# Optimization experiments

Measured on AMD Instinct MI355X. Metric: run time of the kernel, lower is better.

The kernel has to match this reference:

```python
import jax, jax.numpy as jnp
import numpy as np

B, S, D_IN, D_OUT = 4, 2048, 2048, 2048
E, R, TOP_K = 8, 8, 2
ALPHA = 16.0
SCALE = ALPHA / R  # alpha / r


def setup_inputs() -> dict:
    key = jax.random.key(0)
    ks = jax.random.split(key, 6)
    x = jax.random.normal(ks[0], (B, S, D_IN), dtype=jnp.float32)
    # base frozen linear: torch Linear weight [out, in], bias [out]
    W_base = jax.random.normal(ks[1], (D_OUT, D_IN), dtype=jnp.float32) / np.sqrt(D_IN)
    b_base = jax.random.normal(ks[2], (D_OUT,), dtype=jnp.float32) * 0.01
    # router: Linear(in_features, num_experts, bias=False) -> weight [E, in]
    W_router = jax.random.normal(ks[3], (E, D_IN), dtype=jnp.float32) / np.sqrt(D_IN)
    # LoRA experts: A [E, r, in], B [E, out, r] (torch inits B to zero; use small
    # random values so outputs/grads are non-trivial -- math is identical)
    A_w = jax.random.normal(ks[4], (E, R, D_IN), dtype=jnp.float32) / np.sqrt(D_IN)
    B_w = jax.random.normal(ks[5], (E, D_OUT, R), dtype=jnp.float32) * 0.02
    return {"x": x, "W_base": W_base, "b_base": b_base,
            "W_router": W_router, "A_w": A_w, "B_w": B_w}


def reference(x, W_base, b_base, W_router, A_w, B_w):
    # frozen base linear: [B,S,out]
    y = jnp.einsum('bsd,od->bso', x, W_base) + b_base
    # router: logits [B,S,E] -> top-k + softmax over the k selected logits
    logits = jnp.einsum('bsd,ed->bse', x, W_router)
    topk_vals, topk_idx = jax.lax.top_k(logits, TOP_K)       # [B,S,k]
    gates = jax.nn.softmax(topk_vals, axis=-1)               # [B,S,k]
    # all-experts LoRA compute (matches the original dense-stack semantics)
    h = jnp.einsum('bsd,erd->bser', x, A_w)                  # [B,S,E,r]
    expert_outs = jnp.einsum('bser,eor->bseo', h, B_w) * SCALE  # [B,S,E,out]
    # gather the top-k expert outputs and combine with gates
    topk_outs = jnp.take_along_axis(expert_outs, topk_idx[..., None], axis=2)  # [B,S,k,out]
    fused = jnp.sum(topk_outs * gates[..., None], axis=2)    # [B,S,out]
    return y + fused
```

## Files before the change

kernel.cpp:

```cpp
#include <hip/hip_runtime.h>

typedef unsigned short u16;
typedef __attribute__((ext_vector_type(8))) short short8;
typedef __attribute__((ext_vector_type(4))) float f32x4;

#define GLL16(g, l) __builtin_amdgcn_global_load_lds(                         \
    (const __attribute__((address_space(1))) void*)(g),                        \
    (__attribute__((address_space(3))) void*)(l), 16, 0, 0)

__device__ __forceinline__ u16 f2bf(float f) {
  union { float f; unsigned u; } v; v.f = f;
  unsigned u = v.u;
  return (u16)((u + 0x7FFFu + ((u >> 16) & 1u)) >> 16);
}

__global__ __launch_bounds__(512) void k_conv_router(
    const float* __restrict__ x, const float* __restrict__ Wr,
    u16* __restrict__ xbf, float* __restrict__ logits)
{
  __shared__ float wlds[16384];
  {
    const float4* src = (const float4*)Wr;
    float4* dst = (float4*)wlds;
    int t = threadIdx.x;
#pragma unroll
    for (int i = 0; i < 8; ++i) dst[t + i * 512] = src[t + i * 512];
  }
  __syncthreads();
  int wave = threadIdx.x >> 6, lane = threadIdx.x & 63;
  const float4* wv = (const float4*)wlds;
#pragma unroll 1
  for (int s = 0; s < 2; ++s) {
    int tok = blockIdx.x * 16 + wave * 2 + s;
    const float4* xrow = (const float4*)(x + tok * 2048);
    ushort4* orow = (ushort4*)(xbf + tok * 2048);
    float acc[8];
#pragma unroll
    for (int e = 0; e < 8; ++e) acc[e] = 0.f;
#pragma unroll 1
    for (int i = 0; i < 8; ++i) {
      float4 xv = xrow[lane + i * 64];
      ushort4 o;
      o.x = f2bf(xv.x); o.y = f2bf(xv.y);
      o.z = f2bf(xv.z); o.w = f2bf(xv.w);
      orow[lane + i * 64] = o;
#pragma unroll
      for (int e = 0; e < 8; ++e) {
        float4 b = wv[e * 512 + lane + i * 64];
        acc[e] += xv.x * b.x + xv.y * b.y + xv.z * b.z + xv.w * b.w;
      }
    }
#pragma unroll
    for (int e = 0; e < 8; ++e) {
      float v = acc[e];
#pragma unroll
      for (int off = 32; off > 0; off >>= 1) v += __shfl_xor(v, off, 64);
      acc[e] = v;
    }
    if (lane == 0) {
#pragma unroll
      for (int e = 0; e < 8; ++e) logits[tok * 8 + e] = acc[e];
    }
  }
}

__global__ __launch_bounds__(256) void k_convert(
    const float* __restrict__ Wb, const float* __restrict__ Aw,
    const float* __restrict__ Bw,
    u16* __restrict__ wbf, u16* __restrict__ aabf, u16* __restrict__ bmt)
{
  int b = blockIdx.x, t = threadIdx.x;
  if (b < 1024) {
    int tid = b * 256 + t;
    const float4* src = (const float4*)Wb;
    ushort4* dst = (ushort4*)wbf;
#pragma unroll
    for (int i = 0; i < 4; ++i) {
      float4 v = src[tid + i * 262144];
      ushort4 o; o.x = f2bf(v.x); o.y = f2bf(v.y); o.z = f2bf(v.z); o.w = f2bf(v.w);
      dst[tid + i * 262144] = o;
    }
  } else if (b < 1056) {
    int tid = (b - 1024) * 256 + t;
    const float4* src = (const float4*)Aw;
    ushort4* dst = (ushort4*)aabf;
#pragma unroll
    for (int i = 0; i < 4; ++i) {
      float4 v = src[tid + i * 8192];
      ushort4 o; o.x = f2bf(v.x); o.y = f2bf(v.y); o.z = f2bf(v.z); o.w = f2bf(v.w);
      dst[tid + i * 8192] = o;
    }
  } else {
    int n = (b - 1056) * 256 + t;
#pragma unroll
    for (int e = 0; e < 8; ++e) {
      const float4* src = (const float4*)(Bw + e * 16384 + n * 8);
      float4 v0 = src[0], v1 = src[1];
      ushort4 o0, o1;
      o0.x = f2bf(v0.x); o0.y = f2bf(v0.y); o0.z = f2bf(v0.z); o0.w = f2bf(v0.w);
      o1.x = f2bf(v1.x); o1.y = f2bf(v1.y); o1.z = f2bf(v1.z); o1.w = f2bf(v1.w);
      ushort4* dst = (ushort4*)(bmt + n * 64 + e * 8);
      dst[0] = o0; dst[1] = o1;
    }
  }
}

__global__ __launch_bounds__(256) void k_hgemm(
    const u16* __restrict__ xbf, const u16* __restrict__ aabf,
    float* __restrict__ P)
{
  __shared__ u16 As[256 * 64];
  __shared__ u16 Bs[64 * 64];
  int t = threadIdx.x, wave = t >> 6, lane = t & 63;
  int mBase = blockIdx.x * 256;
  int ks = blockIdx.y;
  int fr = lane & 15, fg = lane >> 4;
  int lrow = lane >> 3, lcol = (lane & 7) * 8;
  f32x4 zero = {0.f, 0.f, 0.f, 0.f};
  f32x4 acc[4][4];
#pragma unroll
  for (int i = 0; i < 4; ++i)
#pragma unroll
    for (int j = 0; j < 4; ++j) acc[i][j] = zero;
#pragma unroll 1
  for (int it = 0; it < 4; ++it) {
    int k0 = ks * 256 + it * 64;
    __syncthreads();
#pragma unroll
    for (int cc = 0; cc < 8; ++cc) {
      int c = wave * 8 + cc;
      GLL16(xbf + (mBase + c * 8 + lrow) * 2048 + k0 + lcol, &As[c * 512]);
    }
#pragma unroll
    for (int cc = 0; cc < 2; ++cc) {
      int c = wave * 2 + cc;
      GLL16(aabf + (c * 8 + lrow) * 2048 + k0 + lcol, &Bs[c * 512]);
    }
    __syncthreads();
#pragma unroll
    for (int kk = 0; kk < 2; ++kk) {
      short8 a[4], bfr[4];
#pragma unroll
      for (int i = 0; i < 4; ++i)
        a[i] = *(const short8*)&As[(wave * 64 + i * 16 + fr) * 64 + kk * 32 + fg * 8];
#pragma unroll
      for (int j = 0; j < 4; ++j)
        bfr[j] = *(const short8*)&Bs[(j * 16 + fr) * 64 + kk * 32 + fg * 8];
#pragma unroll
      for (int i = 0; i < 4; ++i)
#pragma unroll
        for (int j = 0; j < 4; ++j)
          acc[i][j] = __builtin_amdgcn_mfma_f32_16x16x32_bf16(a[i], bfr[j], acc[i][j], 0, 0, 0);
    }
  }
#pragma unroll
  for (int i = 0; i < 4; ++i)
#pragma unroll
    for (int j = 0; j < 4; ++j)
#pragma unroll
      for (int r = 0; r < 4; ++r) {
        int m = mBase + wave * 64 + i * 16 + fg * 4 + r;
        int n = j * 16 + fr;
        P[(ks * 8192 + m) * 64 + n] = acc[i][j][r];
      }
}

__global__ __launch_bounds__(256) void k_topk(
    const float* __restrict__ logits, const float* __restrict__ P,
    u16* __restrict__ G)
{
  int t = threadIdx.x, wave = t >> 6, lane = t & 63;
  int tok = blockIdx.x * 4 + wave;
  const float* lg = logits + tok * 8;
  float la[8];
#pragma unroll
  for (int e = 0; e < 8; ++e) la[e] = lg[e];
  float v0 = la[0]; int i0 = 0;
#pragma unroll
  for (int e = 1; e < 8; ++e) { if (la[e] > v0) { v0 = la[e]; i0 = e; } }
  float v1 = -3.4e38f; int i1 = 0;
#pragma unroll
  for (int e = 0; e < 8; ++e) { if (e != i0 && la[e] > v1) { v1 = la[e]; i1 = e; } }
  float ex = expf(v1 - v0);
  float inv = 1.f / (1.f + ex);
  float gate0 = inv, gate1 = ex * inv;
  int e = lane >> 3;
  float h = 0.f;
#pragma unroll
  for (int ks = 0; ks < 8; ++ks) h += P[(ks * 8192 + tok) * 64 + lane];
  float g = (e == i0) ? gate0 : ((e == i1) ? gate1 : 0.f);
  G[tok * 64 + lane] = f2bf(2.0f * g * h);
}

__global__ __launch_bounds__(512, 2) void k_main(
    const u16* __restrict__ xbf, const u16* __restrict__ wbf,
    const u16* __restrict__ G, const u16* __restrict__ BmT,
    const float* __restrict__ bias, float* __restrict__ out)
{
  __shared__ u16 lds[65536];
  const int tid = threadIdx.x;
  const int w = tid >> 6, lane = tid & 63;
  const int fr = lane & 15, fg = lane >> 4;
  const int wr = w >> 2, wc = w & 3;

  const int b0 = blockIdx.x;
  const int wg = (b0 & 7) * 32 + (b0 >> 3);
  const int mBase = (wg >> 3) * 256;
  const int nBase = (wg & 7) * 256;

  const int rl = lane >> 3;
  const int ce = ((lane & 7) ^ rl) << 3;
  const int swz = (fr & 7) << 3;
  const int colk0 = (fg * 8) ^ swz;
  const int colk1 = (32 + fg * 8) ^ swz;
  const int aOff = (wr * 128 + fr) * 64;
  const int bOff = (wc * 64 + fr) * 64;

  f32x4 acc[8][4];
  const f32x4 zero = {0.f, 0.f, 0.f, 0.f};
#pragma unroll
  for (int mi = 0; mi < 8; ++mi)
#pragma unroll
    for (int nj = 0; nj < 4; ++nj) acc[mi][nj] = zero;

  auto STAGE = [&](int s, int which) {
    if (s > 32) return;
    const bool isA = (which < 2);
    const int h = which & 1;
    const u16* src; int ld, k0;
    if (s < 32) { src = isA ? xbf : wbf; ld = 2048; k0 = s * 64; }
    else        { src = isA ? G   : BmT; ld = 64;   k0 = 0;      }
    const int rb = (isA ? mBase : nBase) + h * 128 + w * 8 + rl;
    u16* dst = lds + (isA ? 0 : 32768) + (s & 1) * 16384 + h * 8192 + w * 512;
    GLL16(src + rb * ld + k0 + ce, dst);
    GLL16(src + (rb + 64) * ld + k0 + ce, dst + 4096);
  };

  short8 Aa[2][2], Ab[2][2];
  short8 Bx[4][2], By[4][2];

#define LGKM(N) asm volatile("s_waitcnt lgkmcnt(" #N ")" ::: "memory")
#define VMC(N)  asm volatile("s_waitcnt vmcnt(" #N ")" ::: "memory")
#define BAR()   __builtin_amdgcn_s_barrier()

#define RDA(DST, BUF, MI0)                                                    \
  DST[0][0] = *(const short8*)((BUF) + aOff + (MI0) * 1024 + colk0);          \
  DST[0][1] = *(const short8*)((BUF) + aOff + (MI0) * 1024 + colk1);          \
  DST[1][0] = *(const short8*)((BUF) + aOff + ((MI0) + 1) * 1024 + colk0);    \
  DST[1][1] = *(const short8*)((BUF) + aOff + ((MI0) + 1) * 1024 + colk1);

#define RDB(DST, BUF, NJ0)                                                    \
  DST[(NJ0)][0] = *(const short8*)((BUF) + bOff + (NJ0) * 1024 + colk0);      \
  DST[(NJ0)][1] = *(const short8*)((BUF) + bOff + (NJ0) * 1024 + colk1);      \
  DST[(NJ0)+1][0] = *(const short8*)((BUF) + bOff + ((NJ0)+1) * 1024 + colk0);\
  DST[(NJ0)+1][1] = *(const short8*)((BUF) + bOff + ((NJ0)+1) * 1024 + colk1);

#define MFMA16(AV, BV, MI0)                                                   \
  __builtin_amdgcn_s_setprio(1);                                              \
  _Pragma("unroll")                                                           \
  for (int kk = 0; kk < 2; ++kk)                                              \
    _Pragma("unroll")                                                         \
    for (int q = 0; q < 2; ++q)                                               \
      _Pragma("unroll")                                                       \
      for (int nj = 0; nj < 4; ++nj)                                          \
        acc[(MI0) + q][nj] = __builtin_amdgcn_mfma_f32_16x16x32_bf16(         \
            AV[q][kk], BV[nj][kk], acc[(MI0) + q][nj], 0, 0, 0);              \
  __builtin_amdgcn_s_setprio(0);

#define TILE(T, P, BC, BN)                                                    \
  {                                                                           \
    const u16* Acur = lds + (P) * 16384;                                      \
    const u16* Anxt = lds + (1 - (P)) * 16384;                                \
    const u16* Bnxt = lds + 32768 + (1 - (P)) * 16384;                        \
                                                                      \
    STAGE((T) + 1, 0);                                                        \
    RDA(Ab, Acur, 2)                                                          \
    LGKM(4);                                                                  \
    MFMA16(Aa, BC, 0)                                                         \
    BAR();                                                                    \
                                                                      \
    STAGE((T) + 1, 1);                                                        \
    RDA(Aa, Acur, 4)                                                          \
    LGKM(4);                                                                  \
    MFMA16(Ab, BC, 2)                                                         \
    VMC(4);                                                                   \
    BAR();                                                                    \
                                                                      \
    STAGE((T) + 2, 2);                                                        \
    RDA(Ab, Acur, 6)                                                          \
    RDB(BN, Bnxt, 0)                                                          \
    LGKM(8);                                                                  \
    MFMA16(Aa, BC, 4)                                                         \
    if ((T) == 31) { VMC(0); } else { VMC(2); }                               \
    BAR();                                                                    \
                                                                      \
    STAGE((T) + 2, 3);                                                        \
    RDA(Aa, Anxt, 0)                                                          \
    RDB(BN, Bnxt, 2)                                                          \
    LGKM(8);                                                                  \
    MFMA16(Ab, BC, 6)                                                         \
    BAR();                                                                    \
  }

  STAGE(0, 0); STAGE(0, 1); STAGE(0, 2); STAGE(0, 3);
  STAGE(1, 2); STAGE(1, 3);
  VMC(4);
  BAR();
  {
    const u16* Bb0 = lds + 32768;
    RDB(Bx, Bb0, 0)
    RDB(Bx, Bb0, 2)
    RDA(Aa, lds, 0)
  }

#pragma unroll 1
  for (int tt = 0; tt < 16; ++tt) {
    const int t0 = tt * 2;
    TILE(t0, 0, Bx, By)
    TILE(t0 + 1, 1, By, Bx)
  }

  {
    const u16* Acur = lds;
    RDA(Ab, Acur, 2)
    LGKM(4);
    MFMA16(Aa, Bx, 0)
    RDA(Aa, Acur, 4)
    LGKM(4);
    MFMA16(Ab, Bx, 2)
    RDA(Ab, Acur, 6)
    LGKM(4);
    MFMA16(Aa, Bx, 4)
    LGKM(0);
    MFMA16(Ab, Bx, 6)
  }

#pragma unroll
  for (int nj = 0; nj < 4; ++nj) {
    const int n = nBase + wc * 64 + nj * 16 + fr;
    const float bv = bias[n];
#pragma unroll
    for (int mi = 0; mi < 8; ++mi) {
      const int m = mBase + wr * 128 + mi * 16 + fg * 4;
#pragma unroll
      for (int r = 0; r < 4; ++r)
        out[(m + r) * 2048 + n] = acc[mi][nj][r] + bv;
    }
  }
#undef TILE
#undef MFMA16
#undef RDB
#undef RDA
#undef BAR
#undef VMC
#undef LGKM
}

extern "C" void kernel_launch(void* const* d_in, const int* in_sizes, int n_in,
                              void* d_out, int out_size, void* d_ws, size_t ws_size,
                              hipStream_t stream) {
  const float* x  = (const float*)d_in[0];
  const float* Wb = (const float*)d_in[1];
  const float* bb = (const float*)d_in[2];
  const float* Wr = (const float*)d_in[3];
  const float* Aw = (const float*)d_in[4];
  const float* Bw = (const float*)d_in[5];

  char* ws = (char*)d_ws;
  u16*   xbf  = (u16*)  (ws + 0);
  u16*   wbf  = (u16*)  (ws + 33554432);
  u16*   aabf = (u16*)  (ws + 41943040);
  u16*   bmt  = (u16*)  (ws + 42205184);
  float* lgt  = (float*)(ws + 42467328);
  u16*   G    = (u16*)  (ws + 42729472);
  float* P   = (float*)d_out;
  float* out = (float*)d_out;

  hipLaunchKernelGGL(k_conv_router, dim3(512),    dim3(512), 0, stream, x, Wr, xbf, lgt);
  hipLaunchKernelGGL(k_convert,     dim3(1064),   dim3(256), 0, stream, Wb, Aw, Bw, wbf, aabf, bmt);
  hipLaunchKernelGGL(k_hgemm,       dim3(32, 8),  dim3(256), 0, stream, xbf, aabf, P);
  hipLaunchKernelGGL(k_topk,        dim3(2048),   dim3(256), 0, stream, lgt, P, G);
  hipLaunchKernelGGL(k_main,        dim3(256),    dim3(512), 0, stream, xbf, wbf, G, bmt, bb, out);
}
```

Before: 116.6 us.

## Fuse LoRA A-projection GEMM with top-k gating, drop split-K partials

Replaces the split-K h-GEMM (writing fp32 partials to a scratch buffer) and the separate top-k kernel with one kernel. Each 128-thread block owns 32 tokens and loops over the full K with double-buffered, XOR-swizzled LDS tiles. Routing and gating are computed in the epilogue straight from the accumulators. This removes one launch and the partial-sum write and re-read, but the grid shrinks to 256 small blocks with long serial K loops, which may limit parallelism.

```diff
diff --git a/kernel.cpp b/kernel.cpp
--- a/kernel.cpp
+++ b/kernel.cpp
@@ -105,91 +105,85 @@
   }
 }
 
-__global__ __launch_bounds__(256) void k_hgemm(
+__global__ __launch_bounds__(128) void k_hA(
     const u16* __restrict__ xbf, const u16* __restrict__ aabf,
-    float* __restrict__ P)
+    const float* __restrict__ logits, u16* __restrict__ G)
 {
-  __shared__ u16 As[256 * 64];
-  __shared__ u16 Bs[64 * 64];
-  int t = threadIdx.x, wave = t >> 6, lane = t & 63;
-  int mBase = blockIdx.x * 256;
-  int ks = blockIdx.y;
-  int fr = lane & 15, fg = lane >> 4;
-  int lrow = lane >> 3, lcol = (lane & 7) * 8;
-  f32x4 zero = {0.f, 0.f, 0.f, 0.f};
-  f32x4 acc[4][4];
-#pragma unroll
-  for (int i = 0; i < 4; ++i)
-#pragma unroll
-    for (int j = 0; j < 4; ++j) acc[i][j] = zero;
+  __shared__ u16 As[2][32 * 64];
+  __shared__ u16 Bs[2][64 * 64];
+  const int tid = threadIdx.x, w = tid >> 6, lane = tid & 63;
+  const int fr = lane & 15, fg = lane >> 4;
+  const int rl = lane >> 3;
+  const int ce = ((lane & 7) ^ rl) << 3;
+  const int swz = (fr & 7) << 3;
+  const int colk0 = (fg * 8) ^ swz;
+  const int colk1 = (32 + fg * 8) ^ swz;
+  const int tokBase = blockIdx.x * 32;
+
+  auto STAGE = [&](int s) {
+    const int buf = s & 1, k0 = s * 64;
+    GLL16(xbf + (tokBase + w * 16 + rl) * 2048 + k0 + ce, &As[buf][(w * 16) * 64]);
+    GLL16(xbf + (tokBase + w * 16 + 8 + rl) * 2048 + k0 + ce, &As[buf][(w * 16 + 8) * 64]);
+#pragma unroll
+    for (int c = 0; c < 4; ++c)
+      GLL16(aabf + (w * 32 + c * 8 + rl) * 2048 + k0 + ce, &Bs[buf][(w * 32 + c * 8) * 64]);
+  };
+
+  f32x4 acc[4];
+  const f32x4 zero = {0.f, 0.f, 0.f, 0.f};
+#pragma unroll
+  for (int nj = 0; nj < 4; ++nj) acc[nj] = zero;
+
+  STAGE(0);
+  asm volatile("s_waitcnt vmcnt(0)" ::: "memory");
+  __syncthreads();
+
 #pragma unroll 1
-  for (int it = 0; it < 4; ++it) {
-    int k0 = ks * 256 + it * 64;
+  for (int t = 0; t < 32; ++t) {
+    if (t < 31) STAGE(t + 1);
+    const int buf = t & 1;
+    short8 a[2], bfr[4][2];
+    a[0] = *(const short8*)&As[buf][(w * 16 + fr) * 64 + colk0];
+    a[1] = *(const short8*)&As[buf][(w * 16 + fr) * 64 + colk1];
+#pragma unroll
+    for (int nj = 0; nj < 4; ++nj) {
+      bfr[nj][0] = *(const short8*)&Bs[buf][(nj * 16 + fr) * 64 + colk0];
+      bfr[nj][1] = *(const short8*)&Bs[buf][(nj * 16 + fr) * 64 + colk1];
+    }
+    asm volatile("s_waitcnt lgkmcnt(0)" ::: "memory");
+#pragma unroll
+    for (int kk = 0; kk < 2; ++kk)
+#pragma unroll
+      for (int nj = 0; nj < 4; ++nj)
+        acc[nj] = __builtin_amdgcn_mfma_f32_16x16x32_bf16(a[kk], bfr[nj][kk], acc[nj], 0, 0, 0);
+    asm volatile("s_waitcnt vmcnt(0)" ::: "memory");
     __syncthreads();
-#pragma unroll
-    for (int cc = 0; cc < 8; ++cc) {
-      int c = wave * 8 + cc;
-      GLL16(xbf + (mBase + c * 8 + lrow) * 2048 + k0 + lcol, &As[c * 512]);
-    }
-#pragma unroll
-    for (int cc = 0; cc < 2; ++cc) {
-      int c = wave * 2 + cc;
-      GLL16(aabf + (c * 8 + lrow) * 2048 + k0 + lcol, &Bs[c * 512]);
-    }
-    __syncthreads();
-#pragma unroll
-    for (int kk = 0; kk < 2; ++kk) {
-      short8 a[4], bfr[4];
-#pragma unroll
-      for (int i = 0; i < 4; ++i)
-        a[i] = *(const short8*)&As[(wave * 64 + i * 16 + fr) * 64 + kk * 32 + fg * 8];
-#pragma unroll
-      for (int j = 0; j < 4; ++j)
-        bfr[j] = *(const short8*)&Bs[(j * 16 + fr) * 64 + kk * 32 + fg * 8];
-#pragma unroll
-      for (int i = 0; i < 4; ++i)
-#pragma unroll
-        for (int j = 0; j < 4; ++j)
-          acc[i][j] = __builtin_amdgcn_mfma_f32_16x16x32_bf16(a[i], bfr[j], acc[i][j], 0, 0, 0);
-    }
-  }
-#pragma unroll
-  for (int i = 0; i < 4; ++i)
-#pragma unroll
-    for (int j = 0; j < 4; ++j)
-#pragma unroll
-      for (int r = 0; r < 4; ++r) {
-        int m = mBase + wave * 64 + i * 16 + fg * 4 + r;
-        int n = j * 16 + fr;
-        P[(ks * 8192 + m) * 64 + n] = acc[i][j][r];
-      }
-}
-
-__global__ __launch_bounds__(256) void k_topk(
-    const float* __restrict__ logits, const float* __restrict__ P,
-    u16* __restrict__ G)
-{
-  int t = threadIdx.x, wave = t >> 6, lane = t & 63;
-  int tok = blockIdx.x * 4 + wave;
-  const float* lg = logits + tok * 8;
-  float la[8];
-#pragma unroll
-  for (int e = 0; e < 8; ++e) la[e] = lg[e];
-  float v0 = la[0]; int i0 = 0;
-#pragma unroll
-  for (int e = 1; e < 8; ++e) { if (la[e] > v0) { v0 = la[e]; i0 = e; } }
-  float v1 = -3.4e38f; int i1 = 0;
-#pragma unroll
-  for (int e = 0; e < 8; ++e) { if (e != i0 && la[e] > v1) { v1 = la[e]; i1 = e; } }
-  float ex = expf(v1 - v0);
-  float inv = 1.f / (1.f + ex);
-  float gate0 = inv, gate1 = ex * inv;
-  int e = lane >> 3;
-  float h = 0.f;
-#pragma unroll
-  for (int ks = 0; ks < 8; ++ks) h += P[(ks * 8192 + tok) * 64 + lane];
-  float g = (e == i0) ? gate0 : ((e == i1) ? gate1 : 0.f);
-  G[tok * 64 + lane] = f2bf(2.0f * g * h);
+  }
+
+#pragma unroll
+  for (int r = 0; r < 4; ++r) {
+    const int tok = tokBase + w * 16 + fg * 4 + r;
+    const float* lg = logits + tok * 8;
+    float la[8];
+#pragma unroll
+    for (int e = 0; e < 8; ++e) la[e] = lg[e];
+    float v0 = la[0]; int i0 = 0;
+#pragma unroll
+    for (int e = 1; e < 8; ++e) { if (la[e] > v0) { v0 = la[e]; i0 = e; } }
+    float v1 = -3.4e38f; int i1 = 0;
+#pragma unroll
+    for (int e = 0; e < 8; ++e) { if (e != i0 && la[e] > v1) { v1 = la[e]; i1 = e; } }
+    float ex = expf(v1 - v0);
+    float inv = 1.f / (1.f + ex);
+    float gate0 = inv, gate1 = ex * inv;
+#pragma unroll
+    for (int nj = 0; nj < 4; ++nj) {
+      const int er = nj * 16 + fr;
+      const int e = er >> 3;
+      const float g = (e == i0) ? gate0 : ((e == i1) ? gate1 : 0.f);
+      G[tok * 64 + er] = f2bf(2.0f * g * acc[nj][r]);
+    }
+  }
 }
 
 __global__ __launch_bounds__(512, 2) void k_main(
@@ -373,12 +367,10 @@
   u16*   bmt  = (u16*)  (ws + 42205184);
   float* lgt  = (float*)(ws + 42467328);
   u16*   G    = (u16*)  (ws + 42729472);
-  float* P   = (float*)d_out;
   float* out = (float*)d_out;
 
-  hipLaunchKernelGGL(k_conv_router, dim3(512),    dim3(512), 0, stream, x, Wr, xbf, lgt);
-  hipLaunchKernelGGL(k_convert,     dim3(1064),   dim3(256), 0, stream, Wb, Aw, Bw, wbf, aabf, bmt);
-  hipLaunchKernelGGL(k_hgemm,       dim3(32, 8),  dim3(256), 0, stream, xbf, aabf, P);
-  hipLaunchKernelGGL(k_topk,        dim3(2048),   dim3(256), 0, stream, lgt, P, G);
-  hipLaunchKernelGGL(k_main,        dim3(256),    dim3(512), 0, stream, xbf, wbf, G, bmt, bb, out);
-}
+  hipLaunchKernelGGL(k_conv_router, dim3(512),  dim3(512), 0, stream, x, Wr, xbf, lgt);
+  hipLaunchKernelGGL(k_convert,     dim3(1064), dim3(256), 0, stream, Wb, Aw, Bw, wbf, aabf, bmt);
+  hipLaunchKernelGGL(k_hA,          dim3(256),  dim3(128), 0, stream, xbf, aabf, lgt, G);
+  hipLaunchKernelGGL(k_main,        dim3(256),  dim3(512), 0, stream, xbf, wbf, G, bmt, bb, out);
+}
```

After: 124.3 us. +6.6%, slower.

## Fuse all five stages into one cooperative persistent kernel with grid syncs

Applied to the files above, without the earlier changes.

Merges the router/convert, weight-convert, LoRA A GEMM, top-k gating and main GEMM kernels into a single cooperative kernel launched on 256 blocks, with grid-wide syncs between phases. This removes four kernel launches and their inter-kernel gaps. In exchange, the early phases now run on only 256 blocks of 512 threads, so conversion and the small GEMM lose parallelism, and each grid.sync adds barrier cost. Cooperative launch also requires all 256 blocks to be co-resident.

```diff
diff --git a/kernel.cpp b/kernel.cpp
--- a/kernel.cpp
+++ b/kernel.cpp
@@ -1,4 +1,7 @@
 #include <hip/hip_runtime.h>
+#include <hip/hip_cooperative_groups.h>
+
+namespace cg = cooperative_groups;
 
 typedef unsigned short u16;
 typedef __attribute__((ext_vector_type(8))) short short8;
@@ -14,230 +17,212 @@
   return (u16)((u + 0x7FFFu + ((u >> 16) & 1u)) >> 16);
 }
 
-__global__ __launch_bounds__(512) void k_conv_router(
-    const float* __restrict__ x, const float* __restrict__ Wr,
-    u16* __restrict__ xbf, float* __restrict__ logits)
+__device__ __forceinline__ ushort4 cvt4(float4 v) {
+  ushort4 o; o.x = f2bf(v.x); o.y = f2bf(v.y); o.z = f2bf(v.z); o.w = f2bf(v.w);
+  return o;
+}
+
+__global__ __launch_bounds__(512, 2) void k_fused(
+    const float* __restrict__ x, const float* __restrict__ Wb,
+    const float* __restrict__ bias, const float* __restrict__ Wr,
+    const float* __restrict__ Aw, const float* __restrict__ Bw,
+    u16* __restrict__ xbf, u16* __restrict__ wbf, u16* __restrict__ aabf,
+    u16* __restrict__ bmt, float* __restrict__ lgt, u16* __restrict__ G,
+    float* __restrict__ P, float* __restrict__ out)
 {
-  __shared__ float wlds[16384];
-  {
-    const float4* src = (const float4*)Wr;
-    float4* dst = (float4*)wlds;
-    int t = threadIdx.x;
-#pragma unroll
-    for (int i = 0; i < 8; ++i) dst[t + i * 512] = src[t + i * 512];
-  }
-  __syncthreads();
-  int wave = threadIdx.x >> 6, lane = threadIdx.x & 63;
-  const float4* wv = (const float4*)wlds;
-#pragma unroll 1
-  for (int s = 0; s < 2; ++s) {
-    int tok = blockIdx.x * 16 + wave * 2 + s;
-    const float4* xrow = (const float4*)(x + tok * 2048);
-    ushort4* orow = (ushort4*)(xbf + tok * 2048);
-    float acc[8];
-#pragma unroll
-    for (int e = 0; e < 8; ++e) acc[e] = 0.f;
-#pragma unroll 1
-    for (int i = 0; i < 8; ++i) {
-      float4 xv = xrow[lane + i * 64];
-      ushort4 o;
-      o.x = f2bf(xv.x); o.y = f2bf(xv.y);
-      o.z = f2bf(xv.z); o.w = f2bf(xv.w);
-      orow[lane + i * 64] = o;
-#pragma unroll
-      for (int e = 0; e < 8; ++e) {
-        float4 b = wv[e * 512 + lane + i * 64];
-        acc[e] += xv.x * b.x + xv.y * b.y + xv.z * b.z + xv.w * b.w;
-      }
-    }
-#pragma unroll
-    for (int e = 0; e < 8; ++e) {
-      float v = acc[e];
-#pragma unroll
-      for (int off = 32; off > 0; off >>= 1) v += __shfl_xor(v, off, 64);
-      acc[e] = v;
-    }
-    if (lane == 0) {
-#pragma unroll
-      for (int e = 0; e < 8; ++e) logits[tok * 8 + e] = acc[e];
-    }
-  }
-}
-
-__global__ __launch_bounds__(256) void k_convert(
-    const float* __restrict__ Wb, const float* __restrict__ Aw,
-    const float* __restrict__ Bw,
-    u16* __restrict__ wbf, u16* __restrict__ aabf, u16* __restrict__ bmt)
-{
-  int b = blockIdx.x, t = threadIdx.x;
-  if (b < 1024) {
-    int tid = b * 256 + t;
-    const float4* src = (const float4*)Wb;
-    ushort4* dst = (ushort4*)wbf;
-#pragma unroll
-    for (int i = 0; i < 4; ++i) {
-      float4 v = src[tid + i * 262144];
-      ushort4 o; o.x = f2bf(v.x); o.y = f2bf(v.y); o.z = f2bf(v.z); o.w = f2bf(v.w);
-      dst[tid + i * 262144] = o;
-    }
-  } else if (b < 1056) {
-    int tid = (b - 1024) * 256 + t;
-    const float4* src = (const float4*)Aw;
-    ushort4* dst = (ushort4*)aabf;
-#pragma unroll
-    for (int i = 0; i < 4; ++i) {
-      float4 v = src[tid + i * 8192];
-      ushort4 o; o.x = f2bf(v.x); o.y = f2bf(v.y); o.z = f2bf(v.z); o.w = f2bf(v.w);
-      dst[tid + i * 8192] = o;
-    }
-  } else {
-    int n = (b - 1056) * 256 + t;
-#pragma unroll
-    for (int e = 0; e < 8; ++e) {
-      const float4* src = (const float4*)(Bw + e * 16384 + n * 8);
-      float4 v0 = src[0], v1 = src[1];
-      ushort4 o0, o1;
-      o0.x = f2bf(v0.x); o0.y = f2bf(v0.y); o0.z = f2bf(v0.z); o0.w = f2bf(v0.w);
-      o1.x = f2bf(v1.x); o1.y = f2bf(v1.y); o1.z = f2bf(v1.z); o1.w = f2bf(v1.w);
-      ushort4* dst = (ushort4*)(bmt + n * 64 + e * 8);
-      dst[0] = o0; dst[1] = o1;
-    }
-  }
-}
-
-__global__ __launch_bounds__(256) void k_hgemm(
-    const u16* __restrict__ xbf, const u16* __restrict__ aabf,
-    float* __restrict__ P)
-{
-  __shared__ u16 As[256 * 64];
-  __shared__ u16 Bs[64 * 64];
-  int t = threadIdx.x, wave = t >> 6, lane = t & 63;
-  int mBase = blockIdx.x * 256;
-  int ks = blockIdx.y;
-  int fr = lane & 15, fg = lane >> 4;
-  int lrow = lane >> 3, lcol = (lane & 7) * 8;
-  f32x4 zero = {0.f, 0.f, 0.f, 0.f};
-  f32x4 acc[4][4];
-#pragma unroll
-  for (int i = 0; i < 4; ++i)
-#pragma unroll
-    for (int j = 0; j < 4; ++j) acc[i][j] = zero;
-#pragma unroll 1
-  for (int it = 0; it < 4; ++it) {
-    int k0 = ks * 256 + it * 64;
-    __syncthreads();
-#pragma unroll
-    for (int cc = 0; cc < 8; ++cc) {
-      int c = wave * 8 + cc;
-      GLL16(xbf + (mBase + c * 8 + lrow) * 2048 + k0 + lcol, &As[c * 512]);
-    }
-#pragma unroll
-    for (int cc = 0; cc < 2; ++cc) {
-      int c = wave * 2 + cc;
-      GLL16(aabf + (c * 8 + lrow) * 2048 + k0 + lcol, &Bs[c * 512]);
-    }
-    __syncthreads();
-#pragma unroll
-    for (int kk = 0; kk < 2; ++kk) {
-      short8 a[4], bfr[4];
-#pragma unroll
-      for (int i = 0; i < 4; ++i)
-        a[i] = *(const short8*)&As[(wave * 64 + i * 16 + fr) * 64 + kk * 32 + fg * 8];
-#pragma unroll
-      for (int j = 0; j < 4; ++j)
-        bfr[j] = *(const short8*)&Bs[(j * 16 + fr) * 64 + kk * 32 + fg * 8];
-#pragma unroll
-      for (int i = 0; i < 4; ++i)
-#pragma unroll
-        for (int j = 0; j < 4; ++j)
-          acc[i][j] = __builtin_amdgcn_mfma_f32_16x16x32_bf16(a[i], bfr[j], acc[i][j], 0, 0, 0);
-    }
-  }
-#pragma unroll
-  for (int i = 0; i < 4; ++i)
-#pragma unroll
-    for (int j = 0; j < 4; ++j)
-#pragma unroll
-      for (int r = 0; r < 4; ++r) {
-        int m = mBase + wave * 64 + i * 16 + fg * 4 + r;
-        int n = j * 16 + fr;
-        P[(ks * 8192 + m) * 64 + n] = acc[i][j][r];
-      }
-}
-
-__global__ __launch_bounds__(256) void k_topk(
-    const float* __restrict__ logits, const float* __restrict__ P,
-    u16* __restrict__ G)
-{
-  int t = threadIdx.x, wave = t >> 6, lane = t & 63;
-  int tok = blockIdx.x * 4 + wave;
-  const float* lg = logits + tok * 8;
-  float la[8];
-#pragma unroll
-  for (int e = 0; e < 8; ++e) la[e] = lg[e];
-  float v0 = la[0]; int i0 = 0;
-#pragma unroll
-  for (int e = 1; e < 8; ++e) { if (la[e] > v0) { v0 = la[e]; i0 = e; } }
-  float v1 = -3.4e38f; int i1 = 0;
-#pragma unroll
-  for (int e = 0; e < 8; ++e) { if (e != i0 && la[e] > v1) { v1 = la[e]; i1 = e; } }
-  float ex = expf(v1 - v0);
-  float inv = 1.f / (1.f + ex);
-  float gate0 = inv, gate1 = ex * inv;
-  int e = lane >> 3;
-  float h = 0.f;
-#pragma unroll
-  for (int ks = 0; ks < 8; ++ks) h += P[(ks * 8192 + tok) * 64 + lane];
-  float g = (e == i0) ? gate0 : ((e == i1) ? gate1 : 0.f);
-  G[tok * 64 + lane] = f2bf(2.0f * g * h);
-}
-
-__global__ __launch_bounds__(512, 2) void k_main(
-    const u16* __restrict__ xbf, const u16* __restrict__ wbf,
-    const u16* __restrict__ G, const u16* __restrict__ BmT,
-    const float* __restrict__ bias, float* __restrict__ out)
-{
-  __shared__ u16 lds[65536];
+  __shared__ __align__(16) char smem[131072];
+  cg::grid_group grid = cg::this_grid();
+
   const int tid = threadIdx.x;
   const int w = tid >> 6, lane = tid & 63;
   const int fr = lane & 15, fg = lane >> 4;
-  const int wr = w >> 2, wc = w & 3;
-
-  const int b0 = blockIdx.x;
-  const int wg = (b0 & 7) * 32 + (b0 >> 3);
-  const int mBase = (wg >> 3) * 256;
-  const int nBase = (wg & 7) * 256;
-
   const int rl = lane >> 3;
+  const int lcol = (lane & 7) * 8;
   const int ce = ((lane & 7) ^ rl) << 3;
-  const int swz = (fr & 7) << 3;
-  const int colk0 = (fg * 8) ^ swz;
-  const int colk1 = (32 + fg * 8) ^ swz;
-  const int aOff = (wr * 128 + fr) * 64;
-  const int bOff = (wc * 64 + fr) * 64;
-
-  f32x4 acc[8][4];
-  const f32x4 zero = {0.f, 0.f, 0.f, 0.f};
-#pragma unroll
-  for (int mi = 0; mi < 8; ++mi)
-#pragma unroll
-    for (int nj = 0; nj < 4; ++nj) acc[mi][nj] = zero;
-
-  auto STAGE = [&](int s, int which) {
-    if (s > 32) return;
-    const bool isA = (which < 2);
-    const int h = which & 1;
-    const u16* src; int ld, k0;
-    if (s < 32) { src = isA ? xbf : wbf; ld = 2048; k0 = s * 64; }
-    else        { src = isA ? G   : BmT; ld = 64;   k0 = 0;      }
-    const int rb = (isA ? mBase : nBase) + h * 128 + w * 8 + rl;
-    u16* dst = lds + (isA ? 0 : 32768) + (s & 1) * 16384 + h * 8192 + w * 512;
-    GLL16(src + rb * ld + k0 + ce, dst);
-    GLL16(src + (rb + 64) * ld + k0 + ce, dst + 4096);
-  };
-
-  short8 Aa[2][2], Ab[2][2];
-  short8 Bx[4][2], By[4][2];
+
+  {
+    float* wlds = (float*)smem;
+    {
+      const float4* src = (const float4*)Wr;
+      float4* dst = (float4*)wlds;
+#pragma unroll
+      for (int i = 0; i < 8; ++i) dst[tid + i * 512] = src[tid + i * 512];
+    }
+    __syncthreads();
+    const float4* wv = (const float4*)wlds;
+#pragma unroll 1
+    for (int s = 0; s < 4; ++s) {
+      int tok = blockIdx.x * 32 + w * 4 + s;
+      const float4* xrow = (const float4*)(x + tok * 2048);
+      ushort4* orow = (ushort4*)(xbf + tok * 2048);
+      float acc[8];
+#pragma unroll
+      for (int e = 0; e < 8; ++e) acc[e] = 0.f;
+#pragma unroll 1
+      for (int i = 0; i < 8; ++i) {
+        float4 xv = xrow[lane + i * 64];
+        orow[lane + i * 64] = cvt4(xv);
+#pragma unroll
+        for (int e = 0; e < 8; ++e) {
+          float4 b = wv[e * 512 + lane + i * 64];
+          acc[e] += xv.x * b.x + xv.y * b.y + xv.z * b.z + xv.w * b.w;
+        }
+      }
+#pragma unroll
+      for (int e = 0; e < 8; ++e) {
+        float v = acc[e];
+#pragma unroll
+        for (int off = 32; off > 0; off >>= 1) v += __shfl_xor(v, off, 64);
+        acc[e] = v;
+      }
+      if (lane == 0) {
+#pragma unroll
+        for (int e = 0; e < 8; ++e) lgt[tok * 8 + e] = acc[e];
+      }
+    }
+    const int tidg = blockIdx.x * 512 + tid;
+    {
+      const float4* src = (const float4*)Wb;
+      ushort4* dst = (ushort4*)wbf;
+#pragma unroll
+      for (int i = 0; i < 8; ++i) {
+        dst[tidg + i * 131072] = cvt4(src[tidg + i * 131072]);
+      }
+    }
+    if (tidg < 32768) {
+      ((ushort4*)aabf)[tidg] = cvt4(((const float4*)Aw)[tidg]);
+    }
+    if (tidg < 2048) {
+      const int n = tidg;
+#pragma unroll
+      for (int e = 0; e < 8; ++e) {
+        const float4* src = (const float4*)(Bw + e * 16384 + n * 8);
+        ushort4* dst = (ushort4*)(bmt + n * 64 + e * 8);
+        dst[0] = cvt4(src[0]);
+        dst[1] = cvt4(src[1]);
+      }
+    }
+  }
+  __threadfence();
+  grid.sync();
+
+  {
+    u16* As = (u16*)smem;
+    u16* Bs = (u16*)(smem + 32768);
+    const int mBase = (blockIdx.x >> 3) * 256;
+    const int ks = blockIdx.x & 7;
+    f32x4 acc[2][4];
+    const f32x4 zero = {0.f, 0.f, 0.f, 0.f};
+#pragma unroll
+    for (int i = 0; i < 2; ++i)
+#pragma unroll
+      for (int j = 0; j < 4; ++j) acc[i][j] = zero;
+#pragma unroll 1
+    for (int it = 0; it < 4; ++it) {
+      const int k0 = ks * 256 + it * 64;
+      __syncthreads();
+#pragma unroll
+      for (int cc = 0; cc < 4; ++cc) {
+        const int c = w * 4 + cc;
+        GLL16(xbf + (mBase + c * 8 + rl) * 2048 + k0 + lcol, As + c * 512);
+      }
+      GLL16(aabf + (w * 8 + rl) * 2048 + k0 + lcol, Bs + w * 512);
+      __syncthreads();
+#pragma unroll
+      for (int kk = 0; kk < 2; ++kk) {
+        short8 a[2], bfr[4];
+#pragma unroll
+        for (int i = 0; i < 2; ++i)
+          a[i] = *(const short8*)&As[(w * 32 + i * 16 + fr) * 64 + kk * 32 + fg * 8];
+#pragma unroll
+        for (int j = 0; j < 4; ++j)
+          bfr[j] = *(const short8*)&Bs[(j * 16 + fr) * 64 + kk * 32 + fg * 8];
+#pragma unroll
+        for (int i = 0; i < 2; ++i)
+#pragma unroll
+          for (int j = 0; j < 4; ++j)
+            acc[i][j] = __builtin_amdgcn_mfma_f32_16x16x32_bf16(a[i], bfr[j], acc[i][j], 0, 0, 0);
+      }
+    }
+#pragma unroll
+    for (int i = 0; i < 2; ++i)
+#pragma unroll
+      for (int j = 0; j < 4; ++j)
+#pragma unroll
+        for (int r = 0; r < 4; ++r) {
+          const int m = mBase + w * 32 + i * 16 + fg * 4 + r;
+          const int n = j * 16 + fr;
+          P[(ks * 8192 + m) * 64 + n] = acc[i][j][r];
+        }
+  }
+  __threadfence();
+  grid.sync();
+
+  {
+#pragma unroll 1
+    for (int s = 0; s < 4; ++s) {
+      const int tok = blockIdx.x * 32 + w * 4 + s;
+      const float* lg = lgt + tok * 8;
+      float la[8];
+#pragma unroll
+      for (int e = 0; e < 8; ++e) la[e] = lg[e];
+      float v0 = la[0]; int i0 = 0;
+#pragma unroll
+      for (int e = 1; e < 8; ++e) { if (la[e] > v0) { v0 = la[e]; i0 = e; } }
+      float v1 = -3.4e38f; int i1 = 0;
+#pragma unroll
+      for (int e = 0; e < 8; ++e) { if (e != i0 && la[e] > v1) { v1 = la[e]; i1 = e; } }
+      const float ex = expf(v1 - v0);
+      const float inv = 1.f / (1.f + ex);
+      const float gate0 = inv, gate1 = ex * inv;
+      const int e = lane >> 3;
+      float h = 0.f;
+#pragma unroll
+      for (int ks = 0; ks < 8; ++ks) h += P[(ks * 8192 + tok) * 64 + lane];
+      const float g = (e == i0) ? gate0 : ((e == i1) ? gate1 : 0.f);
+      G[tok * 64 + lane] = f2bf(2.0f * g * h);
+    }
+  }
+  __threadfence();
+  grid.sync();
+
+  {
+    u16* ldsb = (u16*)smem;
+    const int wr = w >> 2, wc = w & 3;
+
+    const int b0 = blockIdx.x;
+    const int wg = (b0 & 7) * 32 + (b0 >> 3);
+    const int mBase = (wg >> 3) * 256;
+    const int nBase = (wg & 7) * 256;
+
+    const int swz = (fr & 7) << 3;
+    const int colk0 = (fg * 8) ^ swz;
+    const int colk1 = (32 + fg * 8) ^ swz;
+    const int aOff = (wr * 128 + fr) * 64;
+    const int bOff = (wc * 64 + fr) * 64;
+
+    f32x4 acc[8][4];
+    const f32x4 zero = {0.f, 0.f, 0.f, 0.f};
+#pragma unroll
+    for (int mi = 0; mi < 8; ++mi)
+#pragma unroll
+      for (int nj = 0; nj < 4; ++nj) acc[mi][nj] = zero;
+
+    auto STAGE = [&](int s, int which) {
+      if (s > 32) return;
+      const bool isA = (which < 2);
+      const int h = which & 1;
+      const u16* src; int ld, k0;
+      if (s < 32) { src = isA ? xbf : wbf; ld = 2048; k0 = s * 64; }
+      else        { src = isA ? G   : bmt; ld = 64;   k0 = 0;      }
+      const int rb = (isA ? mBase : nBase) + h * 128 + w * 8 + rl;
+      u16* dst = ldsb + (isA ? 0 : 32768) + (s & 1) * 16384 + h * 8192 + w * 512;
+      GLL16(src + rb * ld + k0 + ce, dst);
+      GLL16(src + (rb + 64) * ld + k0 + ce, dst + 4096);
+    };
+
+    short8 Aa[2][2], Ab[2][2];
+    short8 Bx[4][2], By[4][2];
 
 #define LGKM(N) asm volatile("s_waitcnt lgkmcnt(" #N ")" ::: "memory")
 #define VMC(N)  asm volatile("s_waitcnt vmcnt(" #N ")" ::: "memory")
@@ -267,11 +252,11 @@
             AV[q][kk], BV[nj][kk], acc[(MI0) + q][nj], 0, 0, 0);              \
   __builtin_amdgcn_s_setprio(0);
 
-#define TILE(T, P, BC, BN)                                                    \
+#define TILE(T, Pp, BC, BN)                                                   \
   {                                                                           \
-    const u16* Acur = lds + (P) * 16384;                                      \
-    const u16* Anxt = lds + (1 - (P)) * 16384;                                \
-    const u16* Bnxt = lds + 32768 + (1 - (P)) * 16384;                        \
+    const u16* Acur = ldsb + (Pp) * 16384;                                    \
+    const u16* Anxt = ldsb + (1 - (Pp)) * 16384;                              \
+    const u16* Bnxt = ldsb + 32768 + (1 - (Pp)) * 16384;                      \
                                                                       \
     STAGE((T) + 1, 0);                                                        \
     RDA(Ab, Acur, 2)                                                          \
@@ -302,51 +287,51 @@
     BAR();                                                                    \
   }
 
-  STAGE(0, 0); STAGE(0, 1); STAGE(0, 2); STAGE(0, 3);
-  STAGE(1, 2); STAGE(1, 3);
-  VMC(4);
-  BAR();
-  {
-    const u16* Bb0 = lds + 32768;
-    RDB(Bx, Bb0, 0)
-    RDB(Bx, Bb0, 2)
-    RDA(Aa, lds, 0)
-  }
-
-#pragma unroll 1
-  for (int tt = 0; tt < 16; ++tt) {
-    const int t0 = tt * 2;
-    TILE(t0, 0, Bx, By)
-    TILE(t0 + 1, 1, By, Bx)
-  }
-
-  {
-    const u16* Acur = lds;
-    RDA(Ab, Acur, 2)
-    LGKM(4);
-    MFMA16(Aa, Bx, 0)
-    RDA(Aa, Acur, 4)
-    LGKM(4);
-    MFMA16(Ab, Bx, 2)
-    RDA(Ab, Acur, 6)
-    LGKM(4);
-    MFMA16(Aa, Bx, 4)
-    LGKM(0);
-    MFMA16(Ab, Bx, 6)
-  }
-
-#pragma unroll
-  for (int nj = 0; nj < 4; ++nj) {
-    const int n = nBase + wc * 64 + nj * 16 + fr;
-    const float bv = bias[n];
-#pragma unroll
-    for (int mi = 0; mi < 8; ++mi) {
-      const int m = mBase + wr * 128 + mi * 16 + fg * 4;
-#pragma unroll
-      for (int r = 0; r < 4; ++r)
-        out[(m + r) * 2048 + n] = acc[mi][nj][r] + bv;
-    }
-  }
+    STAGE(0, 0); STAGE(0, 1); STAGE(0, 2); STAGE(0, 3);
+    STAGE(1, 2); STAGE(1, 3);
+    VMC(4);
+    BAR();
+    {
+      const u16* Bb0 = ldsb + 32768;
+      RDB(Bx, Bb0, 0)
+      RDB(Bx, Bb0, 2)
+      RDA(Aa, ldsb, 0)
+    }
+
+#pragma unroll 1
+    for (int tt = 0; tt < 16; ++tt) {
+      const int t0 = tt * 2;
+      TILE(t0, 0, Bx, By)
+      TILE(t0 + 1, 1, By, Bx)
+    }
+
+    {
+      const u16* Acur = ldsb;
+      RDA(Ab, Acur, 2)
+      LGKM(4);
+      MFMA16(Aa, Bx, 0)
+      RDA(Aa, Acur, 4)
+      LGKM(4);
+      MFMA16(Ab, Bx, 2)
+      RDA(Ab, Acur, 6)
+      LGKM(4);
+      MFMA16(Aa, Bx, 4)
+      LGKM(0);
+      MFMA16(Ab, Bx, 6)
+    }
+
+#pragma unroll
+    for (int nj = 0; nj < 4; ++nj) {
+      const int n = nBase + wc * 64 + nj * 16 + fr;
+      const float bv = bias[n];
+#pragma unroll
+      for (int mi = 0; mi < 8; ++mi) {
+        const int m = mBase + wr * 128 + mi * 16 + fg * 4;
+#pragma unroll
+        for (int r = 0; r < 4; ++r)
+          out[(m + r) * 2048 + n] = acc[mi][nj][r] + bv;
+      }
+    }
 #undef TILE
 #undef MFMA16
 #undef RDB
@@ -354,6 +339,7 @@
 #undef BAR
 #undef VMC
 #undef LGKM
+  }
 }
 
 extern "C" void kernel_launch(void* const* d_in, const int* in_sizes, int n_in,
@@ -376,9 +362,10 @@
   float* P   = (float*)d_out;
   float* out = (float*)d_out;
 
-  hipLaunchKernelGGL(k_conv_router, dim3(512),    dim3(512), 0, stream, x, Wr, xbf, lgt);
-  hipLaunchKernelGGL(k_convert,     dim3(1064),   dim3(256), 0, stream, Wb, Aw, Bw, wbf, aabf, bmt);
-  hipLaunchKernelGGL(k_hgemm,       dim3(32, 8),  dim3(256), 0, stream, xbf, aabf, P);
-  hipLaunchKernelGGL(k_topk,        dim3(2048),   dim3(256), 0, stream, lgt, P, G);
-  hipLaunchKernelGGL(k_main,        dim3(256),    dim3(512), 0, stream, xbf, wbf, G, bmt, bb, out);
+  void* args[] = { (void*)&x, (void*)&Wb, (void*)&bb, (void*)&Wr,
+                   (void*)&Aw, (void*)&Bw,
+                   (void*)&xbf, (void*)&wbf, (void*)&aabf, (void*)&bmt,
+                   (void*)&lgt, (void*)&G, (void*)&P, (void*)&out };
+  hipLaunchCooperativeKernel((const void*)k_fused, dim3(256), dim3(512),
+                             args, 0, stream);
 }
```

After: 371.0 us. 3.18x slower.

## Load B operand directly from global into registers instead of staging through LDS

Applied to the files above, without the earlier changes.

The main GEMM kernel stops staging the weight (B) tiles into shared memory. Each wave now reads its B fragments straight from global memory into registers. Only the activation (A) tiles stay double-buffered in LDS, which halves LDS use and drops two barriers per k-tile. The XCD-aware block-index swizzle is also removed. The trade is per-wave global loads that are uncoalesced and redundant across the two row-waves, plus worse L2 locality without the swizzle.

```diff
diff --git a/kernel.cpp b/kernel.cpp
--- a/kernel.cpp
+++ b/kernel.cpp
@@ -197,16 +197,15 @@
     const u16* __restrict__ G, const u16* __restrict__ BmT,
     const float* __restrict__ bias, float* __restrict__ out)
 {
-  __shared__ u16 lds[65536];
+  __shared__ u16 lds[32768];
   const int tid = threadIdx.x;
   const int w = tid >> 6, lane = tid & 63;
   const int fr = lane & 15, fg = lane >> 4;
   const int wr = w >> 2, wc = w & 3;
 
   const int b0 = blockIdx.x;
-  const int wg = (b0 & 7) * 32 + (b0 >> 3);
-  const int mBase = (wg >> 3) * 256;
-  const int nBase = (wg & 7) * 256;
+  const int mBase = (b0 >> 3) * 256;
+  const int nBase = (b0 & 7) * 256;
 
   const int rl = lane >> 3;
   const int ce = ((lane & 7) ^ rl) << 3;
@@ -214,7 +213,7 @@
   const int colk0 = (fg * 8) ^ swz;
   const int colk1 = (32 + fg * 8) ^ swz;
   const int aOff = (wr * 128 + fr) * 64;
-  const int bOff = (wc * 64 + fr) * 64;
+  const int bRow = nBase + wc * 64 + fr;
 
   f32x4 acc[8][4];
   const f32x4 zero = {0.f, 0.f, 0.f, 0.f};
@@ -223,15 +222,13 @@
 #pragma unroll
     for (int nj = 0; nj < 4; ++nj) acc[mi][nj] = zero;
 
-  auto STAGE = [&](int s, int which) {
+  auto STAGE = [&](int s, int h) {
     if (s > 32) return;
-    const bool isA = (which < 2);
-    const int h = which & 1;
     const u16* src; int ld, k0;
-    if (s < 32) { src = isA ? xbf : wbf; ld = 2048; k0 = s * 64; }
-    else        { src = isA ? G   : BmT; ld = 64;   k0 = 0;      }
-    const int rb = (isA ? mBase : nBase) + h * 128 + w * 8 + rl;
-    u16* dst = lds + (isA ? 0 : 32768) + (s & 1) * 16384 + h * 8192 + w * 512;
+    if (s < 32) { src = xbf; ld = 2048; k0 = s * 64; }
+    else        { src = G;   ld = 64;   k0 = 0;      }
+    const int rb = mBase + h * 128 + w * 8 + rl;
+    u16* dst = lds + (s & 1) * 16384 + h * 8192 + w * 512;
     GLL16(src + rb * ld + k0 + ce, dst);
     GLL16(src + (rb + 64) * ld + k0 + ce, dst + 4096);
   };
@@ -249,11 +246,15 @@
   DST[1][0] = *(const short8*)((BUF) + aOff + ((MI0) + 1) * 1024 + colk0);    \
   DST[1][1] = *(const short8*)((BUF) + aOff + ((MI0) + 1) * 1024 + colk1);
 
-#define RDB(DST, BUF, NJ0)                                                    \
-  DST[(NJ0)][0] = *(const short8*)((BUF) + bOff + (NJ0) * 1024 + colk0);      \
-  DST[(NJ0)][1] = *(const short8*)((BUF) + bOff + (NJ0) * 1024 + colk1);      \
-  DST[(NJ0)+1][0] = *(const short8*)((BUF) + bOff + ((NJ0)+1) * 1024 + colk0);\
-  DST[(NJ0)+1][1] = *(const short8*)((BUF) + bOff + ((NJ0)+1) * 1024 + colk1);
+#define RDBG(DST, SRC, LD, K0, NJ0)                                           \
+  DST[(NJ0)][0] = *(const short8*)((SRC) + (bRow + (NJ0) * 16) * (LD) +       \
+                                   (K0) + fg * 8);                            \
+  DST[(NJ0)][1] = *(const short8*)((SRC) + (bRow + (NJ0) * 16) * (LD) +       \
+                                   (K0) + 32 + fg * 8);                       \
+  DST[(NJ0) + 1][0] = *(const short8*)((SRC) + (bRow + ((NJ0) + 1) * 16) *    \
+                                       (LD) + (K0) + fg * 8);                 \
+  DST[(NJ0) + 1][1] = *(const short8*)((SRC) + (bRow + ((NJ0) + 1) * 16) *    \
+                                       (LD) + (K0) + 32 + fg * 8);
 
 #define MFMA16(AV, BV, MI0)                                                   \
   __builtin_amdgcn_s_setprio(1);                                              \
@@ -271,47 +272,41 @@
   {                                                                           \
     const u16* Acur = lds + (P) * 16384;                                      \
     const u16* Anxt = lds + (1 - (P)) * 16384;                                \
-    const u16* Bnxt = lds + 32768 + (1 - (P)) * 16384;                        \
+    const u16* bns = ((T) + 1 < 32) ? wbf : BmT;                              \
+    const int bld = ((T) + 1 < 32) ? 2048 : 64;                               \
+    const int bk0 = ((T) + 1 < 32) ? ((T) + 1) * 64 : 0;                      \
                                                                       \
     STAGE((T) + 1, 0);                                                        \
     RDA(Ab, Acur, 2)                                                          \
     LGKM(4);                                                                  \
+    VMC(2);                                                                   \
     MFMA16(Aa, BC, 0)                                                         \
-    BAR();                                                                    \
                                                                       \
     STAGE((T) + 1, 1);                                                        \
     RDA(Aa, Acur, 4)                                                          \
     LGKM(4);                                                                  \
     MFMA16(Ab, BC, 2)                                                         \
+                                                                      \
+    RDBG(BN, bns, bld, bk0, 0)                                                \
+    RDA(Ab, Acur, 6)                                                          \
+    LGKM(4);                                                                  \
+    MFMA16(Aa, BC, 4)                                                         \
     VMC(4);                                                                   \
     BAR();                                                                    \
                                                                       \
-    STAGE((T) + 2, 2);                                                        \
-    RDA(Ab, Acur, 6)                                                          \
-    RDB(BN, Bnxt, 0)                                                          \
-    LGKM(8);                                                                  \
-    MFMA16(Aa, BC, 4)                                                         \
-    if ((T) == 31) { VMC(0); } else { VMC(2); }                               \
-    BAR();                                                                    \
-                                                                      \
-    STAGE((T) + 2, 3);                                                        \
+    RDBG(BN, bns, bld, bk0, 2)                                                \
     RDA(Aa, Anxt, 0)                                                          \
-    RDB(BN, Bnxt, 2)                                                          \
-    LGKM(8);                                                                  \
+    LGKM(4);                                                                  \
     MFMA16(Ab, BC, 6)                                                         \
     BAR();                                                                    \
   }
 
-  STAGE(0, 0); STAGE(0, 1); STAGE(0, 2); STAGE(0, 3);
-  STAGE(1, 2); STAGE(1, 3);
-  VMC(4);
+  STAGE(0, 0); STAGE(0, 1);
+  RDBG(Bx, wbf, 2048, 0, 0)
+  RDBG(Bx, wbf, 2048, 0, 2)
+  VMC(8);
   BAR();
-  {
-    const u16* Bb0 = lds + 32768;
-    RDB(Bx, Bb0, 0)
-    RDB(Bx, Bb0, 2)
-    RDA(Aa, lds, 0)
-  }
+  RDA(Aa, lds, 0)
 
 #pragma unroll 1
   for (int tt = 0; tt < 16; ++tt) {
@@ -324,6 +319,7 @@
     const u16* Acur = lds;
     RDA(Ab, Acur, 2)
     LGKM(4);
+    VMC(0);
     MFMA16(Aa, Bx, 0)
     RDA(Aa, Acur, 4)
     LGKM(4);
@@ -349,7 +345,7 @@
   }
 #undef TILE
 #undef MFMA16
-#undef RDB
+#undef RDBG
 #undef RDA
 #undef BAR
 #undef VMC
@@ -376,9 +372,9 @@
   float* P   = (float*)d_out;
   float* out = (float*)d_out;
 
-  hipLaunchKernelGGL(k_conv_router, dim3(512),    dim3(512), 0, stream, x, Wr, xbf, lgt);
-  hipLaunchKernelGGL(k_convert,     dim3(1064),   dim3(256), 0, stream, Wb, Aw, Bw, wbf, aabf, bmt);
-  hipLaunchKernelGGL(k_hgemm,       dim3(32, 8),  dim3(256), 0, stream, xbf, aabf, P);
-  hipLaunchKernelGGL(k_topk,        dim3(2048),   dim3(256), 0, stream, lgt, P, G);
-  hipLaunchKernelGGL(k_main,        dim3(256),    dim3(512), 0, stream, xbf, wbf, G, bmt, bb, out);
-}
+  hipLaunchKernelGGL(k_conv_router, dim3(512),   dim3(512), 0, stream, x, Wr, xbf, lgt);
+  hipLaunchKernelGGL(k_convert,     dim3(1064),  dim3(256), 0, stream, Wb, Aw, Bw, wbf, aabf, bmt);
+  hipLaunchKernelGGL(k_hgemm,       dim3(32, 8), dim3(256), 0, stream, xbf, aabf, P);
+  hipLaunchKernelGGL(k_topk,        dim3(2048),  dim3(256), 0, stream, lgt, P, G);
+  hipLaunchKernelGGL(k_main,        dim3(256),   dim3(512), 0, stream, xbf, wbf, G, bmt, bb, out);
+}
```

Result: slower. 145.5 us (+24.8%).
